# Performance work log

Measured on AMD Instinct MI355X. Metric: run time of the kernel, lower is better.

## Reference

```python
import jax, jax.numpy as jnp
import numpy as np

N, K, DIM = 32768, 8192, 512


def setup_inputs() -> dict:
    key = jax.random.key(0)
    kz, kc = jax.random.split(key)
    z = jax.random.normal(kz, (N, DIM), dtype=jnp.float32)
    # nn.init.uniform_(codebook.weight, -1/K, 1/K)
    codebook = jax.random.uniform(kc, (K, DIM), dtype=jnp.float32, minval=-1.0 / K, maxval=1.0 / K)
    return {"z": z, "codebook": codebook}


def reference(z, codebook):
    # Squared Euclidean distances via ||z||^2 - 2 z.c + ||c||^2 (argmin-equivalent to cdist).
    # z: [N, dim], codebook: [K, dim] -> d2: [N, K]
    z_sq = jnp.sum(z * z, axis=-1, keepdims=True)            # [N, 1]
    c_sq = jnp.sum(codebook * codebook, axis=-1)             # [K]
    cross = jnp.einsum('nd,kd->nk', z, codebook)             # [N, K]
    d2 = z_sq - 2.0 * cross + c_sq
    indices = jnp.argmin(d2, axis=-1)                        # [N] int
    z_q_raw = codebook[indices]                              # embedding lookup, [N, dim]
    # Straight-through estimator: forward = z_q_raw, backward grad flows to z.
    z_q = z + jax.lax.stop_gradient(z_q_raw - z)
    return z_q, indices
```

## Files before the change

### kernel.cpp

```cpp
#include <hip/hip_runtime.h>
#include <cstdint>
#include <cstddef>

constexpr int N_ROWS = 32768;
constexpr int KCODES = 8192;
constexpr int DIMS   = 512;
constexpr int NSEG   = 4;
constexpr int SEGC   = KCODES / NSEG;
constexpr int CAND   = 32;
constexpr float MARGIN = 1e-3f;
constexpr int PAIR_CAP = 1 << 18;
constexpr unsigned SENT = 0xFFFFFFFFu;

typedef _Float16 half8 __attribute__((ext_vector_type(8)));
typedef float    f32x4 __attribute__((ext_vector_type(4)));

__device__ __forceinline__ void gload16(const void* g, void* l) {
  __builtin_amdgcn_global_load_lds(
      (const __attribute__((address_space(1))) void*)g,
      (__attribute__((address_space(3))) void*)l, 16, 0, 0);
}

__device__ __forceinline__ unsigned pack_ds(float d, int code) {
  union { _Float16 h; unsigned short u; } c; c.h = (_Float16)d;
  return ((unsigned)c.u << 16) | (unsigned)code;
}
__device__ __forceinline__ float unpack_d(unsigned e) {
  union { _Float16 h; unsigned short u; } c; c.u = (unsigned short)(e >> 16);
  return (float)c.h;
}

__global__ __launch_bounds__(256) void rowsq_kernel(const float* __restrict__ x,
                                                    float* __restrict__ out) {
  int row  = (blockIdx.x * 256 + threadIdx.x) >> 6;
  int lane = threadIdx.x & 63;
  int blk = lane >> 4, l16 = lane & 15;
  const float* p = x + (size_t)row * DIMS + blk * 128 + l16;
  float A[8];
  #pragma unroll
  for (int j = 0; j < 8; ++j) { float v = p[16 * j]; A[j] = __fmul_rn(v, v); }
  float u = __fadd_rn(__fadd_rn(__fadd_rn(A[0], A[1]), __fadd_rn(A[2], A[3])),
                      __fadd_rn(__fadd_rn(A[4], A[5]), __fadd_rn(A[6], A[7])));
  u = __fadd_rn(u, __shfl_xor(u, 8, 64));
  u = __fadd_rn(u, __shfl_xor(u, 4, 64));
  u = __fadd_rn(u, __shfl_xor(u, 2, 64));
  u = __fadd_rn(u, __shfl_xor(u, 1, 64));
  u = __fadd_rn(u, __shfl_xor(u, 16, 64));
  u = __fadd_rn(u, __shfl_xor(u, 32, 64));
  if (lane == 0) out[row] = u;
}

__global__ __launch_bounds__(256) void cvt_cb_kernel(const float* __restrict__ cb,
                                                     _Float16* __restrict__ chs) {
  int i = blockIdx.x * 256 + threadIdx.x;
  float4 v = ((const float4*)cb)[i];
  union { _Float16 h[4]; uint2 u; } p;
  p.h[0] = (_Float16)(v.x * 2048.0f);
  p.h[1] = (_Float16)(v.y * 2048.0f);
  p.h[2] = (_Float16)(v.z * 2048.0f);
  p.h[3] = (_Float16)(v.w * 2048.0f);
  ((uint2*)chs)[i] = p.u;
}
__global__ __launch_bounds__(256) void cvt_z_kernel(const float* __restrict__ z,
                                                    _Float16* __restrict__ zh) {
  int i = blockIdx.x * 256 + threadIdx.x;
  float4 v = ((const float4*)z)[i];
  union { _Float16 h[4]; uint2 u; } p;
  p.h[0] = (_Float16)v.x; p.h[1] = (_Float16)v.y;
  p.h[2] = (_Float16)v.z; p.h[3] = (_Float16)v.w;
  ((uint2*)zh)[i] = p.u;
}

template <bool ZH>
__global__ __launch_bounds__(512, 4) void vq_mfma_kernel(
    const float* __restrict__ z, const _Float16* __restrict__ zh,
    const _Float16* __restrict__ chs, const float* __restrict__ csq,
    unsigned* __restrict__ cand_g, int* __restrict__ cnt_g) {
  __shared__ __align__(16) _Float16 Ah[128 * 64];
  __shared__ __align__(16) _Float16 Bh[128 * 64];
  __shared__ unsigned rowmin_u[128];
  __shared__ int cnt[128];
  __shared__ unsigned char dropped[128];
  __shared__ unsigned cand[128 * CAND];

  const int tid  = threadIdx.x;
  const int seg  = blockIdx.x & (NSEG - 1);
  const int m0   = (blockIdx.x >> 2) * 128;
  const int nt0  = seg * SEGC;
  const int wave = tid >> 6, lane = tid & 63;
  const int wm = wave >> 2, wn = wave & 3;
  const int q = lane >> 4, r = lane & 15;

  const int lrow = lane >> 3;
  const int lcol = ((lane & 7) ^ lrow) << 4;
  const int s_r  = (r & 7) << 4;

  if (tid < 128) { rowmin_u[tid] = 0x7f800000u; cnt[tid] = 0; dropped[tid] = 0; }
  __syncthreads();

  for (int t = 0; t < SEGC / 128; ++t) {
    const int nt = nt0 + t * 128;
    f32x4 acc[4][2];
    #pragma unroll
    for (int mf = 0; mf < 4; ++mf)
      #pragma unroll
      for (int nf = 0; nf < 2; ++nf) acc[mf][nf] = (f32x4){0.f, 0.f, 0.f, 0.f};

    for (int kc = 0; kc < DIMS / 64; ++kc) {
      const int k0 = kc * 64;
      if (ZH) {
        #pragma unroll
        for (int i = 0; i < 2; ++i) {
          const int rw = wave * 16 + i * 8;
          gload16((const char*)zh + ((size_t)(m0 + rw + lrow) * DIMS + k0) * 2 + lcol,
                  (char*)Ah + rw * 128);
          gload16((const char*)chs + ((size_t)(nt + rw + lrow) * DIMS + k0) * 2 + lcol,
                  (char*)Bh + rw * 128);
        }
      } else {
        #pragma unroll
        for (int i = 0; i < 2; ++i) {
          const int cc = i * 512 + tid;
          const int rw = cc >> 3, cs = cc & 7;
          const float* src = z + (size_t)(m0 + rw) * DIMS + k0 + ((cs ^ (rw & 7)) << 3);
          float4 v0 = ((const float4*)src)[0], v1 = ((const float4*)src)[1];
          union { _Float16 h[8]; uint4 u; } p;
          p.h[0] = (_Float16)v0.x; p.h[1] = (_Float16)v0.y;
          p.h[2] = (_Float16)v0.z; p.h[3] = (_Float16)v0.w;
          p.h[4] = (_Float16)v1.x; p.h[5] = (_Float16)v1.y;
          p.h[6] = (_Float16)v1.z; p.h[7] = (_Float16)v1.w;
          *(uint4*)((char*)Ah + rw * 128 + cs * 16) = p.u;
        }
        #pragma unroll
        for (int i = 0; i < 2; ++i) {
          const int rw = wave * 16 + i * 8;
          gload16((const char*)chs + ((size_t)(nt + rw + lrow) * DIMS + k0) * 2 + lcol,
                  (char*)Bh + rw * 128);
        }
      }
      __syncthreads();
      #pragma unroll
      for (int ks = 0; ks < 2; ++ks) {
        const int bb = ks * 64 + q * 16;
        half8 af[4], bf[2];
        #pragma unroll
        for (int mf = 0; mf < 4; ++mf)
          af[mf] = *(const half8*)((const char*)Ah +
                     (wm * 64 + mf * 16 + r) * 128 + (bb ^ s_r));
        #pragma unroll
        for (int nf = 0; nf < 2; ++nf)
          bf[nf] = *(const half8*)((const char*)Bh +
                     (wn * 32 + nf * 16 + r) * 128 + (bb ^ s_r));
        #pragma unroll
        for (int mf = 0; mf < 4; ++mf)
          #pragma unroll
          for (int nf = 0; nf < 2; ++nf)
            acc[mf][nf] = __builtin_amdgcn_mfma_f32_16x16x32_f16(
                af[mf], bf[nf], acc[mf][nf], 0, 0, 0);
      }
      __syncthreads();
    }

    float cs[2];
    #pragma unroll
    for (int nf = 0; nf < 2; ++nf) cs[nf] = csq[nt + wn * 32 + nf * 16 + r];
    float m4[4][4];
    #pragma unroll
    for (int mf = 0; mf < 4; ++mf)
      #pragma unroll
      for (int reg = 0; reg < 4; ++reg) {
        float mn = INFINITY;
        #pragma unroll
        for (int nf = 0; nf < 2; ++nf)
          mn = fminf(mn, __fmaf_rn(-0.0009765625f, acc[mf][nf][reg], cs[nf]));
        m4[mf][reg] = mn;
      }
    #pragma unroll
    for (int mf = 0; mf < 4; ++mf)
      #pragma unroll
      for (int reg = 0; reg < 4; ++reg) {
        float v = m4[mf][reg];
        v = fminf(v, __shfl_xor(v, 1, 64));
        v = fminf(v, __shfl_xor(v, 2, 64));
        v = fminf(v, __shfl_xor(v, 4, 64));
        v = fminf(v, __shfl_xor(v, 8, 64));
        m4[mf][reg] = v;
      }
    if (r == 0) {
      #pragma unroll
      for (int mf = 0; mf < 4; ++mf)
        #pragma unroll
        for (int reg = 0; reg < 4; ++reg)
          atomicMin(&rowmin_u[wm * 64 + mf * 16 + q * 4 + reg],
                    __float_as_uint(m4[mf][reg] + 4.0f));
    }
    __syncthreads();
    #pragma unroll
    for (int mf = 0; mf < 4; ++mf)
      #pragma unroll
      for (int reg = 0; reg < 4; ++reg) {
        const int row = wm * 64 + mf * 16 + q * 4 + reg;
        float thr = __uint_as_float(rowmin_u[row]) - 4.0f + MARGIN;
        #pragma unroll
        for (int nf = 0; nf < 2; ++nf) {
          float d = __fmaf_rn(-0.0009765625f, acc[mf][nf][reg], cs[nf]);
          if (d <= thr) {
            int slot = atomicAdd(&cnt[row], 1);
            if (slot < CAND)
              cand[row * CAND + slot] = pack_ds(d, nt + wn * 32 + nf * 16 + r);
          }
        }
      }
    if ((t & 1) == 1 || t == (SEGC / 128 - 1)) {
      __syncthreads();
      if (tid < 128) {
        const int raw = cnt[tid];
        const int m = raw < CAND ? raw : CAND;
        if (raw > CAND) dropped[tid] = 1;
        const float thr = __uint_as_float(rowmin_u[tid]) - 4.0f + MARGIN;
        int k = 0;
        for (int i = 0; i < m; ++i) {
          unsigned e = cand[tid * CAND + i];
          if (unpack_d(e) <= thr) cand[tid * CAND + k++] = e;
        }
        cnt[tid] = k;
      }
      __syncthreads();
    }
  }
  __syncthreads();
  if (tid < 128)
    cnt_g[(size_t)seg * N_ROWS + m0 + tid] = dropped[tid] ? (CAND + 1) : cnt[tid];
  for (int i = tid; i < 128 * CAND; i += 512)
    cand_g[((size_t)seg * N_ROWS + m0 + i / CAND) * CAND + (i % CAND)] = cand[i];
}

__device__ __forceinline__ float exact_q(const float* zr, const float* cr,
                                         float zsr, float csr) {
  float s1 = 0.f;
  for (int k = 0; k < 384; k += 8) {
    float4 a0 = *(const float4*)(zr + k), a1 = *(const float4*)(zr + k + 4);
    float4 b0 = *(const float4*)(cr + k), b1 = *(const float4*)(cr + k + 4);
    s1 = __fmaf_rn(a0.x, b0.x, s1); s1 = __fmaf_rn(a0.y, b0.y, s1);
    s1 = __fmaf_rn(a0.z, b0.z, s1); s1 = __fmaf_rn(a0.w, b0.w, s1);
    s1 = __fmaf_rn(a1.x, b1.x, s1); s1 = __fmaf_rn(a1.y, b1.y, s1);
    s1 = __fmaf_rn(a1.z, b1.z, s1); s1 = __fmaf_rn(a1.w, b1.w, s1);
  }
  float s2 = 0.f;
  for (int k = 384; k < 512; k += 8) {
    float4 a0 = *(const float4*)(zr + k), a1 = *(const float4*)(zr + k + 4);
    float4 b0 = *(const float4*)(cr + k), b1 = *(const float4*)(cr + k + 4);
    s2 = __fmaf_rn(a0.x, b0.x, s2); s2 = __fmaf_rn(a0.y, b0.y, s2);
    s2 = __fmaf_rn(a0.z, b0.z, s2); s2 = __fmaf_rn(a0.w, b0.w, s2);
    s2 = __fmaf_rn(a1.x, b1.x, s2); s2 = __fmaf_rn(a1.y, b1.y, s2);
    s2 = __fmaf_rn(a1.z, b1.z, s2); s2 = __fmaf_rn(a1.w, b1.w, s2);
  }
  float cross = __fadd_rn(s1, s2);
  return __fadd_rn(__fmaf_rn(-2.f, cross, zsr), csr);
}

__global__ __launch_bounds__(256) void select_kernel(
    const int* __restrict__ cnt_g, const unsigned* __restrict__ cand_g,
    unsigned long long* __restrict__ best, unsigned* __restrict__ pairs,
    int* __restrict__ meta, int* __restrict__ ovf) {
  const int row  = blockIdx.x * 256 + threadIdx.x;
  const int lane = threadIdx.x & 63;
  int c[NSEG]; bool over = false; int tot = 0;
  #pragma unroll
  for (int s = 0; s < NSEG; ++s) {
    c[s] = cnt_g[(size_t)s * N_ROWS + row];
    if (c[s] > CAND) over = true;
    tot += c[s];
  }
  if (tot == 0) over = true;
  unsigned long long bkey = ~0ULL;
  int need = 0;
  float thr = 0.f;
  if (!over) {
    float gm = INFINITY;
    #pragma unroll
    for (int s = 0; s < NSEG; ++s)
      for (int j = 0; j < c[s]; ++j)
        gm = fminf(gm, unpack_d(cand_g[((size_t)s * N_ROWS + row) * CAND + j]));
    thr = gm + MARGIN;
    int k = 0; unsigned first = 0;
    #pragma unroll
    for (int s = 0; s < NSEG; ++s)
      for (int j = 0; j < c[s]; ++j) {
        unsigned e = cand_g[((size_t)s * N_ROWS + row) * CAND + j];
        if (unpack_d(e) <= thr) { if (k == 0) first = e; ++k; }
      }
    if (k == 1) bkey = (unsigned long long)(first & 0x1FFFu);
    else need = k;
  }
  best[row] = bkey;
  int pre = need;
  #pragma unroll
  for (int off = 1; off < 64; off <<= 1) {
    int v = __shfl_up(pre, off, 64);
    if (lane >= off) pre += v;
  }
  int wtot = __shfl(pre, 63, 64);
  int base = 0;
  if (lane == 63 && wtot > 0) base = atomicAdd(&meta[0], wtot);
  base = __shfl(base, 63, 64);
  const int my0 = base + pre - need;
  bool row_ovf = over;
  if (need > 0) {
    if (my0 + need > PAIR_CAP) {
      row_ovf = true;
      for (int j = 0; j < need; ++j) {
        int s = my0 + j;
        if (s < PAIR_CAP) pairs[s] = SENT;
      }
    } else {
      int kk = 0;
      #pragma unroll
      for (int s = 0; s < NSEG; ++s)
        for (int j = 0; j < c[s]; ++j) {
          unsigned e = cand_g[((size_t)s * N_ROWS + row) * CAND + j];
          if (unpack_d(e) <= thr)
            pairs[my0 + kk++] = ((unsigned)row << 13) | (e & 0x1FFFu);
        }
    }
  }
  if (row_ovf) { int s = atomicAdd(&meta[1], 1); ovf[s] = row; }
}

__global__ __launch_bounds__(256) void pairs_kernel(
    const float* __restrict__ z, const float* __restrict__ cb,
    const float* __restrict__ zsq, const float* __restrict__ csq,
    const unsigned* __restrict__ pairs, const int* __restrict__ meta,
    unsigned long long* __restrict__ best) {
  int n = meta[0];
  if (n > PAIR_CAP) n = PAIR_CAP;
  const int i = blockIdx.x * 256 + threadIdx.x;
  if (i >= n) return;
  const unsigned p = pairs[i];
  if (p == SENT) return;
  const int row = (int)(p >> 13), code = (int)(p & 8191u);
  const float qv = exact_q(z + (size_t)row * DIMS, cb + (size_t)code * DIMS,
                           zsq[row], csq[code]);
  const unsigned long long key =
      ((unsigned long long)__float_as_uint(qv) << 32) | (unsigned)code;
  atomicMin(&best[row], key);
}

__global__ __launch_bounds__(256) void fallback_kernel(
    const float* __restrict__ z, const float* __restrict__ cb,
    const float* __restrict__ zsq, const float* __restrict__ csq,
    const int* __restrict__ ovf, const int* __restrict__ meta,
    unsigned long long* __restrict__ best) {
  __shared__ float sc[KCODES];
  __shared__ float zrow[DIMS];
  __shared__ unsigned bmin;
  const int n = meta[1];
  for (int wi = blockIdx.x; wi < n; wi += gridDim.x) {
    const int row = ovf[wi];
    for (int i = threadIdx.x; i < DIMS; i += 256)
      zrow[i] = z[(size_t)row * DIMS + i];
    if (threadIdx.x == 0) bmin = 0x7f800000u;
    __syncthreads();
    const int g = threadIdx.x >> 3;
    const int j = threadIdx.x & 7;
    float lmin = INFINITY;
    for (int c = g; c < KCODES; c += 32) {
      const float* cr = cb + (size_t)c * DIMS;
      float s = 0.f;
      #pragma unroll
      for (int i = 0; i < 16; ++i) {
        float4 a = *(const float4*)(&zrow[j * 4 + i * 32]);
        float4 b = *(const float4*)(cr + j * 4 + i * 32);
        s = __fmaf_rn(a.x, b.x, s); s = __fmaf_rn(a.y, b.y, s);
        s = __fmaf_rn(a.z, b.z, s); s = __fmaf_rn(a.w, b.w, s);
      }
      s += __shfl_xor(s, 1, 64);
      s += __shfl_xor(s, 2, 64);
      s += __shfl_xor(s, 4, 64);
      float d = __fmaf_rn(-2.f, s, csq[c]);
      if (j == 0) sc[c] = d;
      lmin = fminf(lmin, d);
    }
    atomicMin(&bmin, __float_as_uint(lmin + 4.0f));
    __syncthreads();
    const float thr = __uint_as_float(bmin) - 4.0f + 5e-4f;
    const float zsr = zsq[row];
    const float* zr = z + (size_t)row * DIMS;
    for (int c = threadIdx.x; c < KCODES; c += 256) {
      if (sc[c] <= thr) {
        float qv = exact_q(zr, cb + (size_t)c * DIMS, zsr, csq[c]);
        unsigned long long key =
            ((unsigned long long)__float_as_uint(qv) << 32) | (unsigned)c;
        atomicMin(&best[row], key);
      }
    }
    __syncthreads();
  }
}

__global__ __launch_bounds__(256) void gather_kernel(
    const float* __restrict__ cb, const unsigned long long* __restrict__ best,
    float* __restrict__ zq, float* __restrict__ idx_out) {
  const int wave = threadIdx.x >> 6, lane = threadIdx.x & 63;
  const int row = blockIdx.x * 4 + wave;
  const int code = (int)(unsigned)(best[row] & 0xFFFFFFFFu);
  if (lane == 0) idx_out[row] = (float)code;
  const float4* cbv = (const float4*)(cb + (size_t)code * DIMS);
  float4* zqv = (float4*)(zq + (size_t)row * DIMS);
  zqv[lane]      = cbv[lane];
  zqv[lane + 64] = cbv[lane + 64];
}

extern "C" void kernel_launch(void* const* d_in, const int* in_sizes, int n_in,
                              void* d_out, int out_size, void* d_ws, size_t ws_size,
                              hipStream_t stream) {
  const float* z  = (const float*)d_in[0];
  const float* cb = (const float*)d_in[1];
  float* out     = (float*)d_out;
  float* zq      = out;
  float* idx_out = out + (size_t)N_ROWS * DIMS;

  char* w = (char*)d_ws;
  _Float16* cbh = (_Float16*)w;            w += (size_t)KCODES * DIMS * 2;
  float* zsq = (float*)w;                  w += (size_t)N_ROWS * 4;
  float* csq = (float*)w;                  w += (size_t)KCODES * 4;
  int* cnt_g = (int*)w;                    w += (size_t)NSEG * N_ROWS * 4;
  unsigned* cand_g = (unsigned*)w;         w += (size_t)NSEG * N_ROWS * CAND * 4;
  unsigned long long* best = (unsigned long long*)w; w += (size_t)N_ROWS * 8;
  unsigned* pairs = (unsigned*)w;          w += (size_t)PAIR_CAP * 4;
  int* meta = (int*)w;                     w += 256;
  int* ovf = (int*)w;                      w += (size_t)N_ROWS * 4;
  _Float16* zh = (_Float16*)w;             w += (size_t)N_ROWS * DIMS * 2;
  bool use_zh = ((size_t)(w - (char*)d_ws) <= ws_size);

  hipMemsetAsync(meta, 0, 256, stream);

  rowsq_kernel<<<N_ROWS / 4, 256, 0, stream>>>(z, zsq);
  rowsq_kernel<<<KCODES / 4, 256, 0, stream>>>(cb, csq);
  cvt_cb_kernel<<<KCODES * DIMS / 1024, 256, 0, stream>>>(cb, cbh);
  if (use_zh) {
    cvt_z_kernel<<<N_ROWS * DIMS / 1024, 256, 0, stream>>>(z, zh);
    vq_mfma_kernel<true><<<(N_ROWS / 128) * NSEG, 512, 0, stream>>>(
        z, zh, cbh, csq, cand_g, cnt_g);
  } else {
    vq_mfma_kernel<false><<<(N_ROWS / 128) * NSEG, 512, 0, stream>>>(
        z, nullptr, cbh, csq, cand_g, cnt_g);
  }
  select_kernel<<<N_ROWS / 256, 256, 0, stream>>>(cnt_g, cand_g, best, pairs,
                                                  meta, ovf);
  pairs_kernel<<<PAIR_CAP / 256, 256, 0, stream>>>(z, cb, zsq, csq, pairs,
                                                   meta, best);
  fallback_kernel<<<512, 256, 0, stream>>>(z, cb, zsq, csq, ovf, meta, best);
  gather_kernel<<<N_ROWS / 4, 256, 0, stream>>>(cb, best, zq, idx_out);
}
```

Measured before the change: 745.5 us.

## Double-buffer LDS tiles with 32-wide K chunks to overlap loads and MFMA

Replaces the single 64-wide K staging buffer with two 32-wide ping-pong buffers for A and B. The loads for the next K chunk, including the first chunk of the next code tile, are issued before computing on the current buffer. The goal is to hide global-to-LDS latency behind MFMA work and to avoid the double barrier per chunk. The LDS swizzle and read offsets change to match the 64-byte rows. The cost is a barrier for every 32-wide chunk and a different bank-conflict pattern.

New measurement: 759.5 us. About the same (+1.9%).

```diff
diff --git a/kernel.cpp b/kernel.cpp
--- a/kernel.cpp
+++ b/kernel.cpp
@@ -11,6 +11,8 @@
 constexpr float MARGIN = 1e-3f;
 constexpr int PAIR_CAP = 1 << 18;
 constexpr unsigned SENT = 0xFFFFFFFFu;
+constexpr int NT  = SEGC / 128;
+constexpr int NKC = DIMS / 32;
 
 typedef _Float16 half8 __attribute__((ext_vector_type(8)));
 typedef float    f32x4 __attribute__((ext_vector_type(4)));
@@ -76,8 +78,10 @@
     const float* __restrict__ z, const _Float16* __restrict__ zh,
     const _Float16* __restrict__ chs, const float* __restrict__ csq,
     unsigned* __restrict__ cand_g, int* __restrict__ cnt_g) {
-  __shared__ __align__(16) _Float16 Ah[128 * 64];
-  __shared__ __align__(16) _Float16 Bh[128 * 64];
+  __shared__ __align__(16) _Float16 Ah0[128 * 32];
+  __shared__ __align__(16) _Float16 Ah1[128 * 32];
+  __shared__ __align__(16) _Float16 Bh0[128 * 32];
+  __shared__ __align__(16) _Float16 Bh1[128 * 32];
   __shared__ unsigned rowmin_u[128];
   __shared__ int cnt[128];
   __shared__ unsigned char dropped[128];
@@ -91,66 +95,94 @@
   const int wm = wave >> 2, wn = wave & 3;
   const int q = lane >> 4, r = lane & 15;
 
-  const int lrow = lane >> 3;
-  const int lcol = ((lane & 7) ^ lrow) << 4;
-  const int s_r  = (r & 7) << 4;
+  const int srow = lane >> 2;
+  const int scol = (((lane & 3) ^ (srow & 3)) << 4);
+  const int rdoff = ((q * 16) ^ ((r & 3) << 4));
 
   if (tid < 128) { rowmin_u[tid] = 0x7f800000u; cnt[tid] = 0; dropped[tid] = 0; }
+
+  auto stageA = [&](_Float16* Adst, int kc2) {
+    if (ZH) {
+      gload16((const char*)zh +
+                  ((size_t)(m0 + wave * 16 + srow) * DIMS + kc2 * 32) * 2 + scol,
+              (char*)Adst + wave * 1024);
+    } else {
+      const int rw = tid >> 2, cs = tid & 3;
+      const float* src = z + (size_t)(m0 + rw) * DIMS + kc2 * 32 +
+                         ((cs ^ (rw & 3)) << 3);
+      float4 v0 = ((const float4*)src)[0], v1 = ((const float4*)src)[1];
+      union { _Float16 h[8]; uint4 u; } p;
+      p.h[0] = (_Float16)v0.x; p.h[1] = (_Float16)v0.y;
+      p.h[2] = (_Float16)v0.z; p.h[3] = (_Float16)v0.w;
+      p.h[4] = (_Float16)v1.x; p.h[5] = (_Float16)v1.y;
+      p.h[6] = (_Float16)v1.z; p.h[7] = (_Float16)v1.w;
+      *(uint4*)((char*)Adst + rw * 64 + cs * 16) = p.u;
+    }
+  };
+  auto stageB = [&](_Float16* Bdst, int nt2, int kc2) {
+    gload16((const char*)chs +
+                ((size_t)(nt2 + wave * 16 + srow) * DIMS + kc2 * 32) * 2 + scol,
+            (char*)Bdst + wave * 1024);
+  };
+
+  f32x4 acc[4][2];
+  stageA(Ah0, 0);
+  stageB(Bh0, nt0, 0);
   __syncthreads();
 
-  for (int t = 0; t < SEGC / 128; ++t) {
+  for (int t = 0; t < NT; ++t) {
     const int nt = nt0 + t * 128;
-    f32x4 acc[4][2];
     #pragma unroll
     for (int mf = 0; mf < 4; ++mf)
       #pragma unroll
       for (int nf = 0; nf < 2; ++nf) acc[mf][nf] = (f32x4){0.f, 0.f, 0.f, 0.f};
 
-    for (int kc = 0; kc < DIMS / 64; ++kc) {
-      const int k0 = kc * 64;
-      if (ZH) {
-        #pragma unroll
-        for (int i = 0; i < 2; ++i) {
-          const int rw = wave * 16 + i * 8;
-          gload16((const char*)zh + ((size_t)(m0 + rw + lrow) * DIMS + k0) * 2 + lcol,
-                  (char*)Ah + rw * 128);
-          gload16((const char*)chs + ((size_t)(nt + rw + lrow) * DIMS + k0) * 2 + lcol,
-                  (char*)Bh + rw * 128);
+    #pragma unroll 1
+    for (int kc = 0; kc < NKC; kc += 2) {
+      {
+        const int flat = t * NKC + kc + 1;
+        if (flat < NT * NKC) {
+          const int t2 = flat >> 4, kc2 = flat & 15;
+          stageA(Ah1, kc2);
+          stageB(Bh1, nt0 + t2 * 128, kc2);
         }
-      } else {
-        #pragma unroll
-        for (int i = 0; i < 2; ++i) {
-          const int cc = i * 512 + tid;
-          const int rw = cc >> 3, cs = cc & 7;
-          const float* src = z + (size_t)(m0 + rw) * DIMS + k0 + ((cs ^ (rw & 7)) << 3);
-          float4 v0 = ((const float4*)src)[0], v1 = ((const float4*)src)[1];
-          union { _Float16 h[8]; uint4 u; } p;
-          p.h[0] = (_Float16)v0.x; p.h[1] = (_Float16)v0.y;
-          p.h[2] = (_Float16)v0.z; p.h[3] = (_Float16)v0.w;
-          p.h[4] = (_Float16)v1.x; p.h[5] = (_Float16)v1.y;
-          p.h[6] = (_Float16)v1.z; p.h[7] = (_Float16)v1.w;
-          *(uint4*)((char*)Ah + rw * 128 + cs * 16) = p.u;
+      }
+      {
+        half8 af[4], bf[2];
+        #pragma unroll
+        for (int mf = 0; mf < 4; ++mf)
+          af[mf] = *(const half8*)((const char*)Ah0 +
+                     (wm * 64 + mf * 16 + r) * 64 + rdoff);
+        #pragma unroll
+        for (int nf = 0; nf < 2; ++nf)
+          bf[nf] = *(const half8*)((const char*)Bh0 +
+                     (wn * 32 + nf * 16 + r) * 64 + rdoff);
+        #pragma unroll
+        for (int mf = 0; mf < 4; ++mf)
+          #pragma unroll
+          for (int nf = 0; nf < 2; ++nf)
+            acc[mf][nf] = __builtin_amdgcn_mfma_f32_16x16x32_f16(
+                af[mf], bf[nf], acc[mf][nf], 0, 0, 0);
+      }
+      __syncthreads();
+      {
+        const int flat = t * NKC + kc + 2;
+        if (flat < NT * NKC) {
+          const int t2 = flat >> 4, kc2 = flat & 15;
+          stageA(Ah0, kc2);
+          stageB(Bh0, nt0 + t2 * 128, kc2);
         }
-        #pragma unroll
-        for (int i = 0; i < 2; ++i) {
-          const int rw = wave * 16 + i * 8;
-          gload16((const char*)chs + ((size_t)(nt + rw + lrow) * DIMS + k0) * 2 + lcol,
-                  (char*)Bh + rw * 128);
-        }
-      }
-      __syncthreads();
-      #pragma unroll
-      for (int ks = 0; ks < 2; ++ks) {
-        const int bb = ks * 64 + q * 16;
+      }
+      {
         half8 af[4], bf[2];
         #pragma unroll
         for (int mf = 0; mf < 4; ++mf)
-          af[mf] = *(const half8*)((const char*)Ah +
-                     (wm * 64 + mf * 16 + r) * 128 + (bb ^ s_r));
+          af[mf] = *(const half8*)((const char*)Ah1 +
+                     (wm * 64 + mf * 16 + r) * 64 + rdoff);
         #pragma unroll
         for (int nf = 0; nf < 2; ++nf)
-          bf[nf] = *(const half8*)((const char*)Bh +
-                     (wn * 32 + nf * 16 + r) * 128 + (bb ^ s_r));
+          bf[nf] = *(const half8*)((const char*)Bh1 +
+                     (wn * 32 + nf * 16 + r) * 64 + rdoff);
         #pragma unroll
         for (int mf = 0; mf < 4; ++mf)
           #pragma unroll
@@ -211,7 +243,7 @@
           }
         }
       }
-    if ((t & 1) == 1 || t == (SEGC / 128 - 1)) {
+    if ((t & 1) == 1 || t == (NT - 1)) {
       __syncthreads();
       if (tid < 128) {
         const int raw = cnt[tid];
```
